# Kernel tuning notes

Measured on AMD Instinct MI355X. Metric: run time of the kernel, lower is better.

## Reference

```python
import jax, jax.numpy as jnp
import numpy as np

N = 100000      # nodes
E = 1600000     # edges
D = 128         # hidden_dim
H = 8           # num_heads
DH = D // H     # per-head dim (out_dim in MultiHeadAttentionLayer)
EPS = 1e-5


def layer_norm(x, g, b):
    mu = jnp.mean(x, axis=-1, keepdims=True)
    var = jnp.var(x, axis=-1, keepdims=True)
    return (x - mu) * jax.lax.rsqrt(var + EPS) * g + b


def setup_inputs() -> dict:
    key = jax.random.key(0)
    ks = jax.random.split(key, 16)
    s = 1.0 / np.sqrt(D)
    inp = {
        "h": jax.random.normal(ks[0], (N, D), jnp.float32),
        "src": jax.random.randint(ks[1], (E,), 0, N, jnp.int32),
        "dst": jax.random.randint(ks[2], (E,), 0, N, jnp.int32),
        # attention projections (use_bias=False)
        "Wq": jax.random.uniform(ks[3], (D, D), jnp.float32, -s, s),
        "Wk": jax.random.uniform(ks[4], (D, D), jnp.float32, -s, s),
        "Wv": jax.random.uniform(ks[5], (D, D), jnp.float32, -s, s),
        # output projection O (bias=True)
        "Wo": jax.random.uniform(ks[6], (D, D), jnp.float32, -s, s),
        "bo": jnp.zeros((D,), jnp.float32),
        # layer norms
        "g1": jnp.ones((D,), jnp.float32),
        "b1": jnp.zeros((D,), jnp.float32),
        "g2": jnp.ones((D,), jnp.float32),
        "b2": jnp.zeros((D,), jnp.float32),
        # FFN
        "W1": jax.random.uniform(ks[7], (D, 2 * D), jnp.float32, -s, s),
        "c1": jnp.zeros((2 * D,), jnp.float32),
        "W2": jax.random.uniform(ks[8], (2 * D, D), jnp.float32, -1.0 / np.sqrt(2 * D), 1.0 / np.sqrt(2 * D)),
        "c2": jnp.zeros((D,), jnp.float32),
    }
    return inp


def reference(h, src, dst, Wq, Wk, Wv, Wo, bo, g1, b1, g2, b2, W1, c1, W2, c2):
    n = h.shape[0]
    Q = (h @ Wq).reshape(n, H, DH)
    K = (h @ Wk).reshape(n, H, DH)
    V = (h @ Wv).reshape(n, H, DH)

    # per-edge score: (K[src] * Q[dst]).sum(-1), scaled exp with clamp
    score = jnp.einsum('ehd,ehd->eh', K[src], Q[dst])          # [E, H]
    score = jnp.exp(jnp.clip(score / np.sqrt(DH), -5.0, 5.0))  # [E, H]

    # scatter-sum aggregation into destination nodes
    wV = jax.ops.segment_sum(V[src] * score[:, :, None], dst, num_segments=n)  # [N, H, DH]
    z = jax.ops.segment_sum(score, dst, num_segments=n)                        # [N, H]

    # possible_empty=True: divide only where z > 0
    zb = z[:, :, None]
    head_out = jnp.where(zb > 0, wV / jnp.where(zb > 0, zb, 1.0), wV)

    a = head_out.reshape(n, D) @ Wo + bo
    hh = layer_norm(h + a, g1, b1)
    ff = jax.nn.relu(hh @ W1 + c1) @ W2 + c2
    return layer_norm(hh + ff, g2, b2)
```

## Files before the change

kernel.cpp:

```cpp
#include <hip/hip_runtime.h>
#include <hip/hip_bf16.h>

#define D 128

typedef __attribute__((ext_vector_type(8))) short short8;
typedef __attribute__((ext_vector_type(4))) float float4v;
typedef __attribute__((ext_vector_type(2))) float float2v;

__device__ __forceinline__ float4v mfma16(short8 a, short8 b, float4v c) {
  return __builtin_amdgcn_mfma_f32_16x16x32_bf16(a, b, c, 0, 0, 0);
}
__device__ __forceinline__ float b2f(__hip_bfloat16 x) { return __bfloat162float(x); }
__device__ __forceinline__ __hip_bfloat16 f2b(float x) { return __float2bfloat16(x); }
__device__ __forceinline__ unsigned short f2b_bits(float x) {
  __hip_bfloat16 h = __float2bfloat16(x);
  return *reinterpret_cast<unsigned short*>(&h);
}

__device__ __forceinline__ float ldf(const float* p, size_t i) { return p[i]; }
__device__ __forceinline__ float ldf(const __hip_bfloat16* p, size_t i) { return b2f(p[i]); }
__device__ __forceinline__ void stf(float* p, size_t i, float v) { p[i] = v; }
__device__ __forceinline__ void stf(__hip_bfloat16* p, size_t i, float v) { p[i] = f2b(v); }

__device__ __forceinline__ void bar_lds() {
  asm volatile("s_waitcnt lgkmcnt(0)\n\ts_barrier" ::: "memory");
}

__device__ __forceinline__ float2v up2(unsigned w) {
  float2v r;
  r.x = __uint_as_float(w << 16);
  r.y = __uint_as_float(w & 0xffff0000u);
  return r;
}
__device__ __forceinline__ unsigned char f2fp8(float x) {
  int r = __builtin_amdgcn_cvt_pk_fp8_f32(x, x, 0, false);
  return (unsigned char)(r & 0xff);
}
__device__ __forceinline__ float2v cvt2lo(unsigned w) {
  return __builtin_amdgcn_cvt_pk_f32_fp8(w, false);
}
__device__ __forceinline__ float2v cvt2hi(unsigned w) {
  return __builtin_amdgcn_cvt_pk_f32_fp8(w, true);
}

__device__ __forceinline__ short8 cvt8(float4 u0, float4 u1) {
  short8 a;
  a[0] = (short)f2b_bits(u0.x); a[1] = (short)f2b_bits(u0.y);
  a[2] = (short)f2b_bits(u0.z); a[3] = (short)f2b_bits(u0.w);
  a[4] = (short)f2b_bits(u1.x); a[5] = (short)f2b_bits(u1.y);
  a[6] = (short)f2b_bits(u1.z); a[7] = (short)f2b_bits(u1.w);
  return a;
}

__global__ void k_cast_w(const float* __restrict__ wq, const float* __restrict__ wk,
                         const float* __restrict__ wv, const float* __restrict__ wo,
                         const float* __restrict__ w1, const float* __restrict__ w2,
                         __hip_bfloat16* __restrict__ oq, __hip_bfloat16* __restrict__ ok,
                         __hip_bfloat16* __restrict__ ov, __hip_bfloat16* __restrict__ oo,
                         __hip_bfloat16* __restrict__ o1, __hip_bfloat16* __restrict__ o2) {
  int i = blockIdx.x * 256 + threadIdx.x;
  if (i < 65536) {
    int m = i & 16383;
    int which = i >> 14;
    const float* s = (which == 0) ? wq : (which == 1) ? wk : (which == 2) ? wv : wo;
    __hip_bfloat16* o = (which == 0) ? oq : (which == 1) ? ok : (which == 2) ? ov : oo;
    int j = m & 7, t2 = m >> 3;
    int col = t2 & 127, cq = t2 >> 7;
    o[m] = f2b(s[((cq >> 2) * 32 + (cq & 3) * 8 + j) * 128 + col]);
  } else if (i < 98304) {
    int m = i - 65536;
    int j = m & 7, t2 = m >> 3;
    int col = t2 & 255, cq = t2 >> 8;
    o1[m] = f2b(w1[((cq >> 2) * 32 + (cq & 3) * 8 + j) * 256 + col]);
  } else {
    int m = i - 98304;
    int j = m & 7, t2 = m >> 3;
    int col = t2 & 127, cq = t2 >> 7;
    o2[m] = f2b(w2[((cq >> 2) * 32 + (cq & 3) * 8 + j) * 128 + col]);
  }
}

#define MAXB 512

__global__ void k_bhist(const int* __restrict__ dst, int* __restrict__ bh, int E) {
  __shared__ int cnt[MAXB];
  for (int i = threadIdx.x; i < MAXB; i += 256) cnt[i] = 0;
  __syncthreads();
  for (int e = blockIdx.x * 256 + threadIdx.x; e < E; e += gridDim.x * 256)
    atomicAdd(&cnt[dst[e] >> 8], 1);
  __syncthreads();
  for (int i = threadIdx.x; i < MAXB; i += 256)
    if (cnt[i]) atomicAdd(&bh[i], cnt[i]);
}

__global__ void k_bscan(const int* __restrict__ bh, int* __restrict__ bbase,
                        int* __restrict__ bcur, int B) {
  __shared__ int sd[MAXB];
  int t = threadIdx.x;
  int v = (t < B) ? bh[t] : 0;
  sd[t] = v;
  __syncthreads();
  for (int o = 1; o < MAXB; o <<= 1) {
    int x = (t >= o) ? sd[t - o] : 0;
    __syncthreads();
    sd[t] += x;
    __syncthreads();
  }
  if (t < B) {
    int e = sd[t] - v;
    bbase[t] = e;
    bcur[t] = e;
  }
}

__global__ __launch_bounds__(256) void k_bin(const int* __restrict__ src,
                                             const int* __restrict__ dst,
                                             int* __restrict__ bcur,
                                             uint2* __restrict__ binned, int E) {
  __shared__ int cnt[MAXB];
  __shared__ int base[MAXB];
  const int t = threadIdx.x;
  const int e0 = blockIdx.x * 4096;
  for (int i = t; i < MAXB; i += 256) cnt[i] = 0;
  __syncthreads();
  int myb[16], myr[16], ms[16], md[16];
#pragma unroll
  for (int j = 0; j < 16; ++j) {
    int e = e0 + j * 256 + t;
    if (e < E) {
      int d = dst[e];
      ms[j] = src[e];
      md[j] = d;
      int b = d >> 8;
      myb[j] = b;
      myr[j] = atomicAdd(&cnt[b], 1);
    } else {
      myb[j] = -1;
    }
  }
  __syncthreads();
  for (int i = t; i < MAXB; i += 256)
    base[i] = cnt[i] ? atomicAdd(&bcur[i], cnt[i]) : 0;
  __syncthreads();
#pragma unroll
  for (int j = 0; j < 16; ++j)
    if (myb[j] >= 0)
      binned[(size_t)base[myb[j]] + myr[j]] = make_uint2((unsigned)ms[j], (unsigned)md[j]);
}

__global__ __launch_bounds__(256) void k_fine(const uint2* __restrict__ binned,
                                              const int* __restrict__ bh,
                                              const int* __restrict__ bbase,
                                              int* __restrict__ deg,
                                              int* __restrict__ offs,
                                              int* __restrict__ csr, int N) {
  __shared__ int cnt[256];
  __shared__ int cur[256];
  __shared__ int sd[256];
  const int b = blockIdx.x, t = threadIdx.x;
  const int node0 = b << 8;
  cnt[t] = 0;
  __syncthreads();
  const int s0 = bbase[b], len = bh[b];
  for (int i = t; i < len; i += 256) atomicAdd(&cnt[binned[(size_t)s0 + i].y & 255], 1);
  __syncthreads();
  int v = cnt[t];
  sd[t] = v;
  __syncthreads();
  for (int o = 1; o < 256; o <<= 1) {
    int x = (t >= o) ? sd[t - o] : 0;
    __syncthreads();
    sd[t] += x;
    __syncthreads();
  }
  int excl = sd[t] - v;
  cur[t] = excl;
  int node = node0 + t;
  if (node < N) {
    deg[node] = v;
    offs[node] = s0 + excl;
  }
  __syncthreads();
  for (int i = t; i < len; i += 256) {
    uint2 ed = binned[(size_t)s0 + i];
    int p = atomicAdd(&cur[ed.y & 255], 1);
    csr[s0 + p] = (int)ed.x;
  }
}

__global__ __launch_bounds__(512) void gemm_qkv5(const float* __restrict__ A,
                                                 const uint4* __restrict__ wqF,
                                                 const uint4* __restrict__ wkF,
                                                 const uint4* __restrict__ wvF,
                                                 __hip_bfloat16* __restrict__ Q,
                                                 unsigned char* __restrict__ KV8,
                                                 int Nrow) {
  __shared__ short W[3 * 16384];
  const int t = threadIdx.x;
  {
    uint4* W4 = (uint4*)W;
    for (int i = t; i < 2048; i += 512) {
      W4[i] = wqF[i];
      W4[i + 2048] = wkF[i];
      W4[i + 4096] = wvF[i];
    }
  }
  __syncthreads();
  const int lane = t & 63;
  const int ct = t >> 6;
  const int n = lane & 15, quad = lane >> 4;
  const int fbase = quad * 128 + ct * 16 + n;
  const int ntiles = Nrow >> 4;
  const int koff = ct * 32 + ((n >> 3) << 4) + (n & 7);
  int rt = blockIdx.x;
  if (rt >= ntiles) return;
  float4 u[8];
  {
    const float* Ap = A + (size_t)(rt * 16 + n) * 128 + quad * 8;
#pragma unroll
    for (int c = 0; c < 4; ++c) {
      u[2 * c] = *(const float4*)(Ap + c * 32);
      u[2 * c + 1] = *(const float4*)(Ap + c * 32 + 4);
    }
  }
  while (true) {
    const int rtn = rt + gridDim.x;
    const bool more = rtn < ntiles;
    float4 un[8];
    if (more) {
      const float* Ap = A + (size_t)(rtn * 16 + n) * 128 + quad * 8;
#pragma unroll
      for (int c = 0; c < 4; ++c) {
        un[2 * c] = *(const float4*)(Ap + c * 32);
        un[2 * c + 1] = *(const float4*)(Ap + c * 32 + 4);
      }
    }
    short8 a[4];
#pragma unroll
    for (int c = 0; c < 4; ++c) a[c] = cvt8(u[2 * c], u[2 * c + 1]);
    float4v aq = {0.f, 0.f, 0.f, 0.f}, ak = aq, av = aq;
#pragma unroll
    for (int c = 0; c < 4; ++c) {
      const int fo = (fbase + c * 512) * 8;
      short8 fq = *(const short8*)&W[fo];
      short8 fk = *(const short8*)&W[16384 + fo];
      short8 fv = *(const short8*)&W[32768 + fo];
      aq = mfma16(a[c], fq, aq);
      ak = mfma16(a[c], fk, ak);
      av = mfma16(a[c], fv, av);
    }
#pragma unroll
    for (int r = 0; r < 4; ++r) {
      int grow = rt * 16 + quad * 4 + r;
      Q[(size_t)grow * 128 + ct * 16 + n] = f2b(aq[r]);
      size_t b = (size_t)grow * 256 + koff;
      KV8[b] = f2fp8(ak[r]);
      KV8[b + 8] = f2fp8(av[r]);
    }
    if (!more) break;
#pragma unroll
    for (int i = 0; i < 8; ++i) u[i] = un[i];
    rt = rtn;
  }
}

template <int K, typename TR, typename TO>
__global__ __launch_bounds__(512) void ln_gemm(const short* __restrict__ A,
                                               const uint4* __restrict__ BF4,
                                               const float* __restrict__ bias,
                                               const TR* __restrict__ resid,
                                               const float* __restrict__ gam,
                                               const float* __restrict__ bet,
                                               TO* __restrict__ Out, int Nrow) {
  __shared__ short W[K * 128];
  __shared__ float tile[16][132];
  const int t = threadIdx.x;
  {
    uint4* W4 = (uint4*)W;
    for (int i = t; i < K * 16; i += 512) W4[i] = BF4[i];
  }
  __syncthreads();
  const int lane = t & 63;
  const int ct = t >> 6;
  const int n = lane & 15, quad = lane >> 4;
  const int fbase = quad * 128 + ct * 16 + n;
  float biasv = bias[ct * 16 + n];
  const int row2 = t >> 5, sub = t & 31;
  float ga0 = gam[sub],      ga1 = gam[sub + 32];
  float ga2 = gam[sub + 64], ga3 = gam[sub + 96];
  float be0 = bet[sub],      be1 = bet[sub + 32];
  float be2 = bet[sub + 64], be3 = bet[sub + 96];
  const int ntiles = Nrow >> 4;
  for (int rt = blockIdx.x; rt < ntiles; rt += gridDim.x) {
    const short8* Ap = (const short8*)(A + (size_t)(rt * 16 + n) * K + quad * 8);
    short8 a[K / 32];
    float rs[4];
#pragma unroll
    for (int c = 0; c < K / 32; ++c) a[c] = Ap[c * 4];
#pragma unroll
    for (int r = 0; r < 4; ++r)
      rs[r] = ldf(resid, (size_t)(rt * 16 + quad * 4 + r) * 128 + ct * 16 + n);
    float4v acc = {0.f, 0.f, 0.f, 0.f};
#pragma unroll
    for (int c = 0; c < K / 32; ++c) {
      short8 bf = *(const short8*)&W[(fbase + c * 512) * 8];
      acc = mfma16(a[c], bf, acc);
    }
#pragma unroll
    for (int r = 0; r < 4; ++r)
      tile[quad * 4 + r][ct * 16 + n] = acc[r] + biasv + rs[r];
    bar_lds();
    float x0 = tile[row2][sub], x1 = tile[row2][sub + 32];
    float x2 = tile[row2][sub + 64], x3 = tile[row2][sub + 96];
    float s = x0 + x1 + x2 + x3;
    float s2 = x0 * x0 + x1 * x1 + x2 * x2 + x3 * x3;
#pragma unroll
    for (int o = 16; o >= 1; o >>= 1) {
      s += __shfl_xor(s, o);
      s2 += __shfl_xor(s2, o);
    }
    float mean = s * 0.0078125f;
    float var = s2 * 0.0078125f - mean * mean;
    float rstd = rsqrtf(var + 1e-5f);
    size_t base = (size_t)(rt * 16 + row2) * 128;
    stf(Out, base + sub,      (x0 - mean) * rstd * ga0 + be0);
    stf(Out, base + sub + 32, (x1 - mean) * rstd * ga1 + be1);
    stf(Out, base + sub + 64, (x2 - mean) * rstd * ga2 + be2);
    stf(Out, base + sub + 96, (x3 - mean) * rstd * ga3 + be3);
    bar_lds();
  }
}

__global__ __launch_bounds__(512) void ffn_ln(const short* __restrict__ hh,
                                              const uint4* __restrict__ W1F4,
                                              const float* __restrict__ c1,
                                              const uint4* __restrict__ W2F4,
                                              const float* __restrict__ c2,
                                              const float* __restrict__ gam,
                                              const float* __restrict__ bet,
                                              float* __restrict__ Out, int Nrow) {
  __shared__ short W1[32768];
  __shared__ short W2[32768];
  __shared__ short mid[16][264];
  __shared__ float tile[16][132];
  const int t = threadIdx.x;
  {
    uint4* a4 = (uint4*)W1;
    uint4* b4 = (uint4*)W2;
    for (int i = t; i < 4096; i += 512) {
      a4[i] = W1F4[i];
      b4[i] = W2F4[i];
    }
  }
  __syncthreads();
  const int lane = t & 63;
  const int wv = t >> 6;
  const int n = lane & 15, quad = lane >> 4;
  float b1v0 = c1[(wv * 2) * 16 + n], b1v1 = c1[(wv * 2 + 1) * 16 + n];
  float b2v = c2[wv * 16 + n];
  const int row2 = t >> 5, sub = t & 31;
  float ga0 = gam[sub],      ga1 = gam[sub + 32];
  float ga2 = gam[sub + 64], ga3 = gam[sub + 96];
  float be0 = bet[sub],      be1 = bet[sub + 32];
  float be2 = bet[sub + 64], be3 = bet[sub + 96];
  const int ntiles = Nrow >> 4;
  const __hip_bfloat16* hb = (const __hip_bfloat16*)hh;
  const int f1b0 = quad * 256 + (wv * 2) * 16 + n;
  const int f1b1 = quad * 256 + (wv * 2 + 1) * 16 + n;
  const int f2b = quad * 128 + wv * 16 + n;
  int rt = blockIdx.x;
  if (rt >= ntiles) return;
  short8 a[4];
  __hip_bfloat16 rs[4];
  {
    const short8* Ap = (const short8*)(hh + (size_t)(rt * 16 + n) * 128 + quad * 8);
#pragma unroll
    for (int c = 0; c < 4; ++c) a[c] = Ap[c * 4];
#pragma unroll
    for (int r = 0; r < 4; ++r)
      rs[r] = hb[(size_t)(rt * 16 + quad * 4 + r) * 128 + wv * 16 + n];
  }
  while (true) {
    const int rtn = rt + gridDim.x;
    const bool more = rtn < ntiles;
    short8 an[4];
    __hip_bfloat16 rsn[4];
    if (more) {
      const short8* Ap = (const short8*)(hh + (size_t)(rtn * 16 + n) * 128 + quad * 8);
#pragma unroll
      for (int c = 0; c < 4; ++c) an[c] = Ap[c * 4];
#pragma unroll
      for (int r = 0; r < 4; ++r)
        rsn[r] = hb[(size_t)(rtn * 16 + quad * 4 + r) * 128 + wv * 16 + n];
    }
    float4v a10 = {0.f, 0.f, 0.f, 0.f}, a11 = a10;
#pragma unroll
    for (int c = 0; c < 4; ++c) {
      short8 f1a = *(const short8*)&W1[(f1b0 + c * 1024) * 8];
      short8 f1c = *(const short8*)&W1[(f1b1 + c * 1024) * 8];
      a10 = mfma16(a[c], f1a, a10);
      a11 = mfma16(a[c], f1c, a11);
    }
#pragma unroll
    for (int r = 0; r < 4; ++r) {
      mid[quad * 4 + r][(wv * 2) * 16 + n] = (short)f2b_bits(fmaxf(a10[r] + b1v0, 0.f));
      mid[quad * 4 + r][(wv * 2 + 1) * 16 + n] = (short)f2b_bits(fmaxf(a11[r] + b1v1, 0.f));
    }
    bar_lds();
    float4v acc = {0.f, 0.f, 0.f, 0.f};
#pragma unroll
    for (int c = 0; c < 8; ++c) {
      short8 am = *(const short8*)&mid[n][quad * 8 + c * 32];
      short8 f2 = *(const short8*)&W2[(f2b + c * 512) * 8];
      acc = mfma16(am, f2, acc);
    }
#pragma unroll
    for (int r = 0; r < 4; ++r)
      tile[quad * 4 + r][wv * 16 + n] = acc[r] + b2v + b2f(rs[r]);
    bar_lds();
    float x0 = tile[row2][sub], x1 = tile[row2][sub + 32];
    float x2 = tile[row2][sub + 64], x3 = tile[row2][sub + 96];
    float s = x0 + x1 + x2 + x3;
    float s2 = x0 * x0 + x1 * x1 + x2 * x2 + x3 * x3;
#pragma unroll
    for (int o = 16; o >= 1; o >>= 1) {
      s += __shfl_xor(s, o);
      s2 += __shfl_xor(s2, o);
    }
    float mean = s * 0.0078125f;
    float var = s2 * 0.0078125f - mean * mean;
    float rstd = rsqrtf(var + 1e-5f);
    size_t base = (size_t)(rt * 16 + row2) * 128;
    Out[base + sub]      = (x0 - mean) * rstd * ga0 + be0;
    Out[base + sub + 32] = (x1 - mean) * rstd * ga1 + be1;
    Out[base + sub + 64] = (x2 - mean) * rstd * ga2 + be2;
    Out[base + sub + 96] = (x3 - mean) * rstd * ga3 + be3;
    bar_lds();
    if (!more) break;
#pragma unroll
    for (int c = 0; c < 4; ++c) a[c] = an[c];
#pragma unroll
    for (int r = 0; r < 4; ++r) rs[r] = rsn[r];
    rt = rtn;
  }
}

__global__ __launch_bounds__(256) void attn_agg5(const uint4* __restrict__ Q4,
                                                 const uint4* __restrict__ KV8,
                                                 const int* __restrict__ offs,
                                                 const int* __restrict__ deg,
                                                 const int* __restrict__ csr,
                                                 uint4* __restrict__ AT4, int N) {
  const int lane = threadIdx.x & 63;
  const int wv = threadIdx.x >> 6;
  const int e4 = lane >> 4;
  const int hd = (lane >> 1) & 7;
  const int hf = lane & 1;
  const int kvo = hd * 2 + hf;
  for (int node = blockIdx.x * 4 + wv; node < N; node += gridDim.x * 4) {
    uint4 qa = Q4[(size_t)node * 16 + kvo];
    float2v qv[4];
    qv[0] = up2(qa.x); qv[1] = up2(qa.y); qv[2] = up2(qa.z); qv[3] = up2(qa.w);
    float2v acc[4];
#pragma unroll
    for (int d = 0; d < 4; ++d) acc[d] = (float2v){0.f, 0.f};
    float z = 0.f;
    const int st = offs[node], dg = deg[node];
    if (dg > 0) {
      const int dgm1 = dg - 1;
      int s_cur = csr[st + min(e4, dgm1)];
      int s_nxt = (dg > 4) ? csr[st + min(4 + e4, dgm1)] : s_cur;
      uint4 ckv = KV8[(size_t)s_cur * 16 + kvo];
      int i = 0;
      while (true) {
        const bool more = (i + 4) < dg;
        uint4 nkv;
        int s_fut = s_nxt;
        if (more) {
          nkv = KV8[(size_t)s_nxt * 16 + kvo];
          s_fut = csr[st + min(i + 8 + e4, dgm1)];
        }
        float2v p2 = cvt2lo(ckv.x) * qv[0];
        p2 += cvt2hi(ckv.x) * qv[1];
        p2 += cvt2lo(ckv.y) * qv[2];
        p2 += cvt2hi(ckv.y) * qv[3];
        float p = p2.x + p2.y;
        p += __shfl_xor(p, 1);
        float sc = __expf(fminf(fmaxf(p * 0.25f, -5.f), 5.f));
        sc = ((i + e4) < dg) ? sc : 0.f;
        z += sc;
        float2v sv = {sc, sc};
        acc[0] += cvt2lo(ckv.z) * sv;
        acc[1] += cvt2hi(ckv.z) * sv;
        acc[2] += cvt2lo(ckv.w) * sv;
        acc[3] += cvt2hi(ckv.w) * sv;
        if (!more) break;
        ckv = nkv;
        s_nxt = s_fut;
        i += 4;
      }
    }
#pragma unroll
    for (int m = 16; m <= 32; m <<= 1) {
      z += __shfl_xor(z, m);
#pragma unroll
      for (int d = 0; d < 4; ++d) {
        acc[d].x += __shfl_xor(acc[d].x, m);
        acc[d].y += __shfl_xor(acc[d].y, m);
      }
    }
    if (e4 == 0) {
      float inv = (z > 0.f) ? 1.f / z : 1.f;
      unsigned r[4];
#pragma unroll
      for (int j = 0; j < 4; ++j)
        r[j] = (unsigned)f2b_bits(acc[j].x * inv) |
               ((unsigned)f2b_bits(acc[j].y * inv) << 16);
      AT4[(size_t)node * 16 + kvo] = make_uint4(r[0], r[1], r[2], r[3]);
    }
  }
}

extern "C" void kernel_launch(void* const* d_in, const int* in_sizes, int n_in,
                              void* d_out, int out_size, void* d_ws, size_t ws_size,
                              hipStream_t stream) {
  const float* h = (const float*)d_in[0];
  const int* src = (const int*)d_in[1];
  const int* dst = (const int*)d_in[2];
  const float* Wq = (const float*)d_in[3];
  const float* Wk = (const float*)d_in[4];
  const float* Wv = (const float*)d_in[5];
  const float* Wo = (const float*)d_in[6];
  const float* bo = (const float*)d_in[7];
  const float* g1 = (const float*)d_in[8];
  const float* b1 = (const float*)d_in[9];
  const float* g2 = (const float*)d_in[10];
  const float* b2 = (const float*)d_in[11];
  const float* W1 = (const float*)d_in[12];
  const float* c1 = (const float*)d_in[13];
  const float* W2 = (const float*)d_in[14];
  const float* c2 = (const float*)d_in[15];

  const int N = in_sizes[0] / D;
  const int E = in_sizes[1];
  const int B = (N + 255) >> 8;

  char* p = (char*)d_ws;
  auto carve = [&](size_t bytes) {
    char* r = p;
    p += (bytes + 255) & ~(size_t)255;
    return r;
  };
  short* ATb = (short*)carve((size_t)N * D * 2);
  short* Qb = (short*)carve((size_t)N * D * 2);
  unsigned char* KVb = (unsigned char*)carve((size_t)N * 256);
  short* wq = (short*)carve(16384 * 2);
  short* wk = (short*)carve(16384 * 2);
  short* wv = (short*)carve(16384 * 2);
  short* wo = (short*)carve(16384 * 2);
  short* w1 = (short*)carve(32768 * 2);
  short* w2 = (short*)carve(32768 * 2);
  int* deg = (int*)carve((size_t)N * 4);
  int* offs = (int*)carve((size_t)N * 4);
  int* bh = (int*)carve(MAXB * 4);
  int* bbase = (int*)carve(MAXB * 4);
  int* bcur = (int*)carve(MAXB * 4);
  uint2* binned = (uint2*)carve((size_t)E * 8);
  int* csr = (int*)carve((size_t)E * 4);
  short* hh = Qb;

  hipMemsetAsync(bh, 0, MAXB * 4, stream);
  k_bhist<<<1024, 256, 0, stream>>>(dst, bh, E);
  k_bscan<<<1, MAXB, 0, stream>>>(bh, bbase, bcur, B);
  k_bin<<<(E + 4095) / 4096, 256, 0, stream>>>(src, dst, bcur, binned, E);
  k_fine<<<B, 256, 0, stream>>>(binned, bh, bbase, deg, offs, csr, N);

  k_cast_w<<<512, 256, 0, stream>>>(Wq, Wk, Wv, Wo, W1, W2,
                                    (__hip_bfloat16*)wq, (__hip_bfloat16*)wk,
                                    (__hip_bfloat16*)wv, (__hip_bfloat16*)wo,
                                    (__hip_bfloat16*)w1, (__hip_bfloat16*)w2);

  gemm_qkv5<<<256, 512, 0, stream>>>(h, (const uint4*)wq, (const uint4*)wk,
                                     (const uint4*)wv, (__hip_bfloat16*)Qb, KVb, N);

  attn_agg5<<<(N + 3) >> 2, 256, 0, stream>>>((const uint4*)Qb, (const uint4*)KVb,
                                              offs, deg, csr, (uint4*)ATb, N);

  ln_gemm<128, float, __hip_bfloat16><<<768, 512, 0, stream>>>(
      ATb, (const uint4*)wo, bo, h, g1, b1, (__hip_bfloat16*)hh, N);
  ffn_ln<<<256, 512, 0, stream>>>(hh, (const uint4*)w1, c1, (const uint4*)w2, c2,
                                  g2, b2, (float*)d_out, N);
}
```

Measured before the change: 398.1 us.

## Fuse histogram with weight cast, pack binned edges, double-buffer LDS tiles

Merges the dst-histogram and weight-cast kernels into one launch, which removes a kernel launch. Binned edges are packed into 32 bits (src<<8 | dst&255) instead of uint2, halving binning traffic; this assumes src fits in 24 bits. The QKV GEMM now runs two 512-thread groups per 1024-thread block so each block processes two row tiles, sharing a single LDS weight load. The LN-GEMM and FFN kernels double-buffer their LDS staging tiles so the trailing barrier per iteration can be dropped, at the cost of more LDS use.

```diff
diff --git a/kernel.cpp b/kernel.cpp
--- a/kernel.cpp
+++ b/kernel.cpp
@@ -2,6 +2,7 @@
 #include <hip/hip_bf16.h>
 
 #define D 128
+#define MAXB 512
 
 typedef __attribute__((ext_vector_type(8))) short short8;
 typedef __attribute__((ext_vector_type(4))) float float4v;
@@ -52,13 +53,21 @@
   return a;
 }
 
-__global__ void k_cast_w(const float* __restrict__ wq, const float* __restrict__ wk,
-                         const float* __restrict__ wv, const float* __restrict__ wo,
-                         const float* __restrict__ w1, const float* __restrict__ w2,
-                         __hip_bfloat16* __restrict__ oq, __hip_bfloat16* __restrict__ ok,
-                         __hip_bfloat16* __restrict__ ov, __hip_bfloat16* __restrict__ oo,
-                         __hip_bfloat16* __restrict__ o1, __hip_bfloat16* __restrict__ o2) {
-  int i = blockIdx.x * 256 + threadIdx.x;
+__global__ __launch_bounds__(256) void k_bhist_cast(
+    const int* __restrict__ dst, int* __restrict__ bh, int E,
+    const float* __restrict__ wq, const float* __restrict__ wk,
+    const float* __restrict__ wv, const float* __restrict__ wo,
+    const float* __restrict__ w1, const float* __restrict__ w2,
+    __hip_bfloat16* __restrict__ oq, __hip_bfloat16* __restrict__ ok,
+    __hip_bfloat16* __restrict__ ov, __hip_bfloat16* __restrict__ oo,
+    __hip_bfloat16* __restrict__ o1, __hip_bfloat16* __restrict__ o2) {
+  __shared__ int cnt[MAXB];
+  const int t = threadIdx.x;
+  const int gid = blockIdx.x * 256 + t;
+  for (int i = t; i < MAXB; i += 256) cnt[i] = 0;
+  __syncthreads();
+  for (int e = gid; e < E; e += gridDim.x * 256) atomicAdd(&cnt[dst[e] >> 8], 1);
+  int i = gid;
   if (i < 65536) {
     int m = i & 16383;
     int which = i >> 14;
@@ -72,25 +81,15 @@
     int j = m & 7, t2 = m >> 3;
     int col = t2 & 255, cq = t2 >> 8;
     o1[m] = f2b(w1[((cq >> 2) * 32 + (cq & 3) * 8 + j) * 256 + col]);
-  } else {
+  } else if (i < 131072) {
     int m = i - 98304;
     int j = m & 7, t2 = m >> 3;
     int col = t2 & 127, cq = t2 >> 7;
     o2[m] = f2b(w2[((cq >> 2) * 32 + (cq & 3) * 8 + j) * 128 + col]);
   }
-}
-
-#define MAXB 512
-
-__global__ void k_bhist(const int* __restrict__ dst, int* __restrict__ bh, int E) {
-  __shared__ int cnt[MAXB];
-  for (int i = threadIdx.x; i < MAXB; i += 256) cnt[i] = 0;
-  __syncthreads();
-  for (int e = blockIdx.x * 256 + threadIdx.x; e < E; e += gridDim.x * 256)
-    atomicAdd(&cnt[dst[e] >> 8], 1);
-  __syncthreads();
-  for (int i = threadIdx.x; i < MAXB; i += 256)
-    if (cnt[i]) atomicAdd(&bh[i], cnt[i]);
+  __syncthreads();
+  for (int k = t; k < MAXB; k += 256)
+    if (cnt[k]) atomicAdd(&bh[k], cnt[k]);
 }
 
 __global__ void k_bscan(const int* __restrict__ bh, int* __restrict__ bbase,
@@ -116,21 +115,21 @@
 __global__ __launch_bounds__(256) void k_bin(const int* __restrict__ src,
                                              const int* __restrict__ dst,
                                              int* __restrict__ bcur,
-                                             uint2* __restrict__ binned, int E) {
+                                             unsigned* __restrict__ binned, int E) {
   __shared__ int cnt[MAXB];
   __shared__ int base[MAXB];
   const int t = threadIdx.x;
   const int e0 = blockIdx.x * 4096;
   for (int i = t; i < MAXB; i += 256) cnt[i] = 0;
   __syncthreads();
-  int myb[16], myr[16], ms[16], md[16];
+  int myb[16], myr[16];
+  unsigned pk[16];
 #pragma unroll
   for (int j = 0; j < 16; ++j) {
     int e = e0 + j * 256 + t;
     if (e < E) {
       int d = dst[e];
-      ms[j] = src[e];
-      md[j] = d;
+      pk[j] = ((unsigned)src[e] << 8) | (unsigned)(d & 255);
       int b = d >> 8;
       myb[j] = b;
       myr[j] = atomicAdd(&cnt[b], 1);
@@ -144,11 +143,10 @@
   __syncthreads();
 #pragma unroll
   for (int j = 0; j < 16; ++j)
-    if (myb[j] >= 0)
-      binned[(size_t)base[myb[j]] + myr[j]] = make_uint2((unsigned)ms[j], (unsigned)md[j]);
-}
-
-__global__ __launch_bounds__(256) void k_fine(const uint2* __restrict__ binned,
+    if (myb[j] >= 0) binned[(size_t)base[myb[j]] + myr[j]] = pk[j];
+}
+
+__global__ __launch_bounds__(256) void k_fine(const unsigned* __restrict__ binned,
                                               const int* __restrict__ bh,
                                               const int* __restrict__ bbase,
                                               int* __restrict__ deg,
@@ -162,7 +160,7 @@
   cnt[t] = 0;
   __syncthreads();
   const int s0 = bbase[b], len = bh[b];
-  for (int i = t; i < len; i += 256) atomicAdd(&cnt[binned[(size_t)s0 + i].y & 255], 1);
+  for (int i = t; i < len; i += 256) atomicAdd(&cnt[binned[(size_t)s0 + i] & 255], 1);
   __syncthreads();
   int v = cnt[t];
   sd[t] = v;
@@ -182,37 +180,40 @@
   }
   __syncthreads();
   for (int i = t; i < len; i += 256) {
-    uint2 ed = binned[(size_t)s0 + i];
-    int p = atomicAdd(&cur[ed.y & 255], 1);
-    csr[s0 + p] = (int)ed.x;
-  }
-}
-
-__global__ __launch_bounds__(512) void gemm_qkv5(const float* __restrict__ A,
-                                                 const uint4* __restrict__ wqF,
-                                                 const uint4* __restrict__ wkF,
-                                                 const uint4* __restrict__ wvF,
-                                                 __hip_bfloat16* __restrict__ Q,
-                                                 unsigned char* __restrict__ KV8,
-                                                 int Nrow) {
+    unsigned ed = binned[(size_t)s0 + i];
+    int p = atomicAdd(&cur[ed & 255], 1);
+    csr[s0 + p] = (int)(ed >> 8);
+  }
+}
+
+__global__ __launch_bounds__(1024) void gemm_qkv6(const float* __restrict__ A,
+                                                  const uint4* __restrict__ wqF,
+                                                  const uint4* __restrict__ wkF,
+                                                  const uint4* __restrict__ wvF,
+                                                  __hip_bfloat16* __restrict__ Q,
+                                                  unsigned char* __restrict__ KV8,
+                                                  int Nrow) {
   __shared__ short W[3 * 16384];
   const int t = threadIdx.x;
   {
     uint4* W4 = (uint4*)W;
-    for (int i = t; i < 2048; i += 512) {
+    for (int i = t; i < 2048; i += 1024) {
       W4[i] = wqF[i];
       W4[i + 2048] = wkF[i];
       W4[i + 4096] = wvF[i];
     }
   }
   __syncthreads();
-  const int lane = t & 63;
-  const int ct = t >> 6;
+  const int half = t >> 9;
+  const int th = t & 511;
+  const int lane = th & 63;
+  const int ct = th >> 6;
   const int n = lane & 15, quad = lane >> 4;
   const int fbase = quad * 128 + ct * 16 + n;
   const int ntiles = Nrow >> 4;
   const int koff = ct * 32 + ((n >> 3) << 4) + (n & 7);
-  int rt = blockIdx.x;
+  const int step = gridDim.x * 2;
+  int rt = blockIdx.x * 2 + half;
   if (rt >= ntiles) return;
   float4 u[8];
   {
@@ -224,7 +225,7 @@
     }
   }
   while (true) {
-    const int rtn = rt + gridDim.x;
+    const int rtn = rt + step;
     const bool more = rtn < ntiles;
     float4 un[8];
     if (more) {
@@ -273,7 +274,7 @@
                                                const float* __restrict__ bet,
                                                TO* __restrict__ Out, int Nrow) {
   __shared__ short W[K * 128];
-  __shared__ float tile[16][132];
+  __shared__ float tile[2][16][132];
   const int t = threadIdx.x;
   {
     uint4* W4 = (uint4*)W;
@@ -291,7 +292,8 @@
   float be0 = bet[sub],      be1 = bet[sub + 32];
   float be2 = bet[sub + 64], be3 = bet[sub + 96];
   const int ntiles = Nrow >> 4;
-  for (int rt = blockIdx.x; rt < ntiles; rt += gridDim.x) {
+  int pp = 0;
+  for (int rt = blockIdx.x; rt < ntiles; rt += gridDim.x, pp ^= 1) {
     const short8* Ap = (const short8*)(A + (size_t)(rt * 16 + n) * K + quad * 8);
     short8 a[K / 32];
     float rs[4];
@@ -308,10 +310,10 @@
     }
 #pragma unroll
     for (int r = 0; r < 4; ++r)
-      tile[quad * 4 + r][ct * 16 + n] = acc[r] + biasv + rs[r];
+      tile[pp][quad * 4 + r][ct * 16 + n] = acc[r] + biasv + rs[r];
     bar_lds();
-    float x0 = tile[row2][sub], x1 = tile[row2][sub + 32];
-    float x2 = tile[row2][sub + 64], x3 = tile[row2][sub + 96];
+    float x0 = tile[pp][row2][sub], x1 = tile[pp][row2][sub + 32];
+    float x2 = tile[pp][row2][sub + 64], x3 = tile[pp][row2][sub + 96];
     float s = x0 + x1 + x2 + x3;
     float s2 = x0 * x0 + x1 * x1 + x2 * x2 + x3 * x3;
 #pragma unroll
@@ -327,7 +329,6 @@
     stf(Out, base + sub + 32, (x1 - mean) * rstd * ga1 + be1);
     stf(Out, base + sub + 64, (x2 - mean) * rstd * ga2 + be2);
     stf(Out, base + sub + 96, (x3 - mean) * rstd * ga3 + be3);
-    bar_lds();
   }
 }
 
@@ -341,7 +342,7 @@
                                               float* __restrict__ Out, int Nrow) {
   __shared__ short W1[32768];
   __shared__ short W2[32768];
-  __shared__ short mid[16][264];
+  __shared__ short mid[2][16][264];
   __shared__ float tile[16][132];
   const int t = threadIdx.x;
   {
@@ -380,6 +381,7 @@
     for (int r = 0; r < 4; ++r)
       rs[r] = hb[(size_t)(rt * 16 + quad * 4 + r) * 128 + wv * 16 + n];
   }
+  int mp = 0;
   while (true) {
     const int rtn = rt + gridDim.x;
     const bool more = rtn < ntiles;
@@ -403,14 +405,14 @@
     }
 #pragma unroll
     for (int r = 0; r < 4; ++r) {
-      mid[quad * 4 + r][(wv * 2) * 16 + n] = (short)f2b_bits(fmaxf(a10[r] + b1v0, 0.f));
-      mid[quad * 4 + r][(wv * 2 + 1) * 16 + n] = (short)f2b_bits(fmaxf(a11[r] + b1v1, 0.f));
+      mid[mp][quad * 4 + r][(wv * 2) * 16 + n] = (short)f2b_bits(fmaxf(a10[r] + b1v0, 0.f));
+      mid[mp][quad * 4 + r][(wv * 2 + 1) * 16 + n] = (short)f2b_bits(fmaxf(a11[r] + b1v1, 0.f));
     }
     bar_lds();
     float4v acc = {0.f, 0.f, 0.f, 0.f};
 #pragma unroll
     for (int c = 0; c < 8; ++c) {
-      short8 am = *(const short8*)&mid[n][quad * 8 + c * 32];
+      short8 am = *(const short8*)&mid[mp][n][quad * 8 + c * 32];
       short8 f2 = *(const short8*)&W2[(f2b + c * 512) * 8];
       acc = mfma16(am, f2, acc);
     }
@@ -435,13 +437,13 @@
     Out[base + sub + 32] = (x1 - mean) * rstd * ga1 + be1;
     Out[base + sub + 64] = (x2 - mean) * rstd * ga2 + be2;
     Out[base + sub + 96] = (x3 - mean) * rstd * ga3 + be3;
-    bar_lds();
     if (!more) break;
 #pragma unroll
     for (int c = 0; c < 4; ++c) a[c] = an[c];
 #pragma unroll
     for (int r = 0; r < 4; ++r) rs[r] = rsn[r];
     rt = rtn;
+    mp ^= 1;
   }
 }
 
@@ -565,23 +567,21 @@
   int* bh = (int*)carve(MAXB * 4);
   int* bbase = (int*)carve(MAXB * 4);
   int* bcur = (int*)carve(MAXB * 4);
-  uint2* binned = (uint2*)carve((size_t)E * 8);
+  unsigned* binned = (unsigned*)carve((size_t)E * 4);
   int* csr = (int*)carve((size_t)E * 4);
   short* hh = Qb;
 
   hipMemsetAsync(bh, 0, MAXB * 4, stream);
-  k_bhist<<<1024, 256, 0, stream>>>(dst, bh, E);
+  k_bhist_cast<<<1024, 256, 0, stream>>>(
+      dst, bh, E, Wq, Wk, Wv, Wo, W1, W2,
+      (__hip_bfloat16*)wq, (__hip_bfloat16*)wk, (__hip_bfloat16*)wv,
+      (__hip_bfloat16*)wo, (__hip_bfloat16*)w1, (__hip_bfloat16*)w2);
   k_bscan<<<1, MAXB, 0, stream>>>(bh, bbase, bcur, B);
   k_bin<<<(E + 4095) / 4096, 256, 0, stream>>>(src, dst, bcur, binned, E);
   k_fine<<<B, 256, 0, stream>>>(binned, bh, bbase, deg, offs, csr, N);
 
-  k_cast_w<<<512, 256, 0, stream>>>(Wq, Wk, Wv, Wo, W1, W2,
-                                    (__hip_bfloat16*)wq, (__hip_bfloat16*)wk,
-                                    (__hip_bfloat16*)wv, (__hip_bfloat16*)wo,
-                                    (__hip_bfloat16*)w1, (__hip_bfloat16*)w2);
-
-  gemm_qkv5<<<256, 512, 0, stream>>>(h, (const uint4*)wq, (const uint4*)wk,
-                                     (const uint4*)wv, (__hip_bfloat16*)Qb, KVb, N);
+  gemm_qkv6<<<256, 1024, 0, stream>>>(h, (const uint4*)wq, (const uint4*)wk,
+                                      (const uint4*)wv, (__hip_bfloat16*)Qb, KVb, N);
 
   attn_agg5<<<(N + 3) >> 2, 256, 0, stream>>>((const uint4*)Qb, (const uint4*)KVb,
                                               offs, deg, csr, (uint4*)ATb, N);
```

New measurement: 392.1 us. No clear change (-1.5%).
